# Kernel tuning notes

Hardware: AMD Instinct MI355X
Metric: run time of the kernel (lower is better)

Reference implementation:

```python
import jax, jax.numpy as jnp
import numpy as np

B, F, U, A, H = 8192, 1024, 256, 16, 8  # batch, in_features, units_layer, num_actions, hidden(=8)


def _coagent_layer(x, W0, b0, W1, b1, W2, b2):
    # x: [B, f_in]; stacked weights for U independent tiny MLPs (grouped GEMMs)
    h = jax.nn.relu(jnp.einsum('bf,uhf->buh', x, W0) + b0)   # [B, U, H]
    h = jax.nn.relu(jnp.einsum('buh,ugh->bug', h, W1) + b1)  # [B, U, H]
    q = jnp.einsum('bug,uag->bua', h, W2) + b2               # [B, U, A]
    # greedy action per coagent (epsilon-greedy with greedy=True / epsilon=0)
    return jnp.argmax(q, axis=-1).astype(jnp.float32)        # [B, U]


def setup_inputs() -> dict:
    key = jax.random.key(0)
    ks = jax.random.split(key, 19)
    n = lambda k, shape, fan: (jax.random.normal(k, shape, dtype=jnp.float32)
                               / jnp.sqrt(jnp.float32(fan)))
    return {
        'state': jax.random.normal(ks[0], (B, F), dtype=jnp.float32),
        # coagent layer 0: in_features -> 8 -> 8 -> A, stacked over U units
        'W0_0': n(ks[1], (U, H, F), F), 'b0_0': jnp.zeros((U, H), jnp.float32),
        'W1_0': n(ks[2], (U, H, H), H), 'b1_0': jnp.zeros((U, H), jnp.float32),
        'W2_0': n(ks[3], (U, A, H), H), 'b2_0': jnp.zeros((U, A), jnp.float32),
        # coagent layer 1: units_layer -> 8 -> 8 -> A, stacked over U units
        'W0_1': n(ks[4], (U, H, U), U), 'b0_1': jnp.zeros((U, H), jnp.float32),
        'W1_1': n(ks[5], (U, H, H), H), 'b1_1': jnp.zeros((U, H), jnp.float32),
        'W2_1': n(ks[6], (U, A, H), H), 'b2_1': jnp.zeros((U, A), jnp.float32),
        # Policy head: units_layer -> 8 -> 8 -> 1
        'PW0': n(ks[7], (H, U), U), 'Pb0': jnp.zeros((H,), jnp.float32),
        'PW1': n(ks[8], (H, H), H), 'Pb1': jnp.zeros((H,), jnp.float32),
        'PW2': n(ks[9], (1, H), H), 'Pb2': jnp.zeros((1,), jnp.float32),
    }


def reference(state, W0_0, b0_0, W1_0, b1_0, W2_0, b2_0,
              W0_1, b0_1, W1_1, b1_1, W2_1, b2_1,
              PW0, Pb0, PW1, Pb1, PW2, Pb2):
    a0 = _coagent_layer(state, W0_0, b0_0, W1_0, b1_0, W2_0, b2_0)  # [B, U]
    a1 = _coagent_layer(a0, W0_1, b0_1, W1_1, b1_1, W2_1, b2_1)     # [B, U]
    h = jax.nn.relu(a1 @ PW0.T + Pb0)
    h = jax.nn.relu(h @ PW1.T + Pb1)
    return h @ PW2.T + Pb2  # [B, 1]
```

## Files before the change

### kernel.cpp

```cpp
#include <hip/hip_runtime.h>
#include <cstring>
#include <cstdint>

#define B_TOTAL 8192
#define F_IN    1024
#define U_UNITS 256
#define NACT    16
#define HID     8

typedef float    f32x4  __attribute__((ext_vector_type(4)));
typedef _Float16 half8  __attribute__((ext_vector_type(8)));
typedef _Float16 half4  __attribute__((ext_vector_type(4)));


__global__ __launch_bounds__(256)
void pack3_kernel(const float* __restrict__ s0, _Float16* __restrict__ d0h, _Float16* __restrict__ d0l,
                  const float* __restrict__ s1, _Float16* __restrict__ d1h, _Float16* __restrict__ d1l,
                  const float* __restrict__ s2, _Float16* __restrict__ d2h, _Float16* __restrict__ d2l)
{
    constexpr int NB0 = (B_TOTAL / 16) * (F_IN / 128);
    constexpr int NB1 = (U_UNITS * HID / 16) * (F_IN / 128);
    __shared__ float ls[16 * 132];
    int b = blockIdx.x;
    const float* src; _Float16 *dh, *dl; int K, lg;
    if (b < NB0)            { src = s0; dh = d0h; dl = d0l; K = F_IN;    lg = 3; }
    else if (b < NB0 + NB1) { b -= NB0; src = s1; dh = d1h; dl = d1l; K = F_IN; lg = 3; }
    else                    { b -= NB0 + NB1; src = s2; dh = d2h; dl = d2l; K = U_UNITS; lg = 1; }

    const int tid = threadIdx.x;
    const int mt  = b >> lg;
    const int kb  = b & ((1 << lg) - 1);
    const int r0  = mt * 16;

#pragma unroll
    for (int i = 0; i < 2; ++i) {
        const int e = tid + (i << 8);
        const int row = e >> 5;
        const int c4  = e & 31;
        f32x4 v = *reinterpret_cast<const f32x4*>(
            &src[(size_t)(r0 + row) * K + (kb << 7) + (c4 << 2)]);
        *reinterpret_cast<f32x4*>(&ls[row * 132 + (c4 << 2)]) = v;
    }
    __syncthreads();

    const int k8 = tid >> 4, r = tid & 15;
    float x[8];
#pragma unroll
    for (int j = 0; j < 8; ++j) x[j] = ls[r * 132 + (k8 << 3) + j];
    half8 h, l;
#pragma unroll
    for (int j = 0; j < 8; ++j) {
        h[j] = (_Float16)x[j];
        l[j] = (_Float16)((x[j] - (float)h[j]) * 2048.0f);
    }
    const size_t off = (((size_t)mt * (K >> 5)) + (kb << 2) + (k8 >> 2)) * 512
                     + (size_t)(((k8 & 3) << 4) + r) * 8;
    *reinterpret_cast<half8*>(&dh[off]) = h;
    *reinterpret_cast<half8*>(&dl[off]) = l;
}

constexpr int BM = 128, BN = 128;

template<int K_TOTAL, bool A_SPLIT, bool OUT_TF32>
__global__ __launch_bounds__(256, 2)
void coagent_mfma(const _Float16* __restrict__ Ahg, const _Float16* __restrict__ Alg,
                  const _Float16* __restrict__ Bhg, const _Float16* __restrict__ Blg,
                  const float* __restrict__ b0, const float* __restrict__ W1,
                  const float* __restrict__ b1, const float* __restrict__ W2,
                  const float* __restrict__ b2, void* __restrict__ outp)
{
    struct EpiBufs { float Hs[BM][65]; _Float16 ab[BM * 8]; };
    __shared__ EpiBufs sm;

    constexpr int NTK = K_TOTAL >> 5;
    constexpr size_t TS = (size_t)NTK * 512;

    const int tid  = threadIdx.x;
    const int wave = tid >> 6;
    const int lane = tid & 63;
    const int quad = lane >> 4;
    const int l15  = lane & 15;
    const int wm   = (wave >> 1) * 64;
    const int m0   = blockIdx.y * BM;
    const int n0   = blockIdx.x * BN;

    const int at = (wave >> 1) * 4;
    const int bt = (wave & 1) * 4;

    const _Float16* Ah0 = Ahg + ((size_t)((m0 >> 4) + at)) * TS + lane * 8;
    const _Float16* Al0 = A_SPLIT ? (Alg + ((size_t)((m0 >> 4) + at)) * TS + lane * 8) : nullptr;
    const _Float16* Bh0 = Bhg + ((size_t)((n0 >> 4) + bt)) * TS + lane * 8;
    const _Float16* Bl0 = Blg + ((size_t)((n0 >> 4) + bt)) * TS + lane * 8;

    f32x4 acc1[4][4];
    f32x4 acc2[4][4];
#pragma unroll
    for (int i = 0; i < 4; ++i)
#pragma unroll
        for (int j = 0; j < 4; ++j) { acc1[i][j] = {0.f,0.f,0.f,0.f}; acc2[i][j] = {0.f,0.f,0.f,0.f}; }

    for (int kt = 0; kt < NTK; ++kt) {
        const size_t ko = (size_t)kt * 512;
        half8 af[4], bf[4], xa[4], xb[4];
#pragma unroll
        for (int mt = 0; mt < 4; ++mt)
            af[mt] = *reinterpret_cast<const half8*>(Ah0 + mt * TS + ko);
#pragma unroll
        for (int nt = 0; nt < 4; ++nt)
            bf[nt] = *reinterpret_cast<const half8*>(Bh0 + nt * TS + ko);
        if (A_SPLIT) {
#pragma unroll
            for (int mt = 0; mt < 4; ++mt)
                xa[mt] = *reinterpret_cast<const half8*>(Al0 + mt * TS + ko);
        }
#pragma unroll
        for (int nt = 0; nt < 4; ++nt)
            xb[nt] = *reinterpret_cast<const half8*>(Bl0 + nt * TS + ko);

#pragma unroll
        for (int mt = 0; mt < 4; ++mt)
#pragma unroll
            for (int nt = 0; nt < 4; ++nt)
                acc1[mt][nt] = __builtin_amdgcn_mfma_f32_16x16x32_f16(af[mt], bf[nt], acc1[mt][nt], 0, 0, 0);
        if (A_SPLIT) {
#pragma unroll
            for (int mt = 0; mt < 4; ++mt)
#pragma unroll
                for (int nt = 0; nt < 4; ++nt)
                    acc2[mt][nt] = __builtin_amdgcn_mfma_f32_16x16x32_f16(xa[mt], bf[nt], acc2[mt][nt], 0, 0, 0);
        }
#pragma unroll
        for (int mt = 0; mt < 4; ++mt)
#pragma unroll
            for (int nt = 0; nt < 4; ++nt)
                acc2[mt][nt] = __builtin_amdgcn_mfma_f32_16x16x32_f16(af[mt], xb[nt], acc2[mt][nt], 0, 0, 0);
    }

    const int ubase = n0 >> 3;
    for (int half = 0; half < 2; ++half) {
        __syncthreads();
        if ((wave & 1) == half) {
#pragma unroll
            for (int mt = 0; mt < 4; ++mt)
#pragma unroll
                for (int nt = 0; nt < 4; ++nt)
#pragma unroll
                    for (int r = 0; r < 4; ++r)
                        sm.Hs[wm + mt * 16 + quad * 4 + r][nt * 16 + l15] =
                            acc1[mt][nt][r] + acc2[mt][nt][r] * (1.0f / 2048.0f);
        }
        __syncthreads();
#pragma unroll
        for (int p = 0; p < 4; ++p) {
            const int pair = (p << 8) + tid;
            const int ul = pair >> 7;
            const int bl = pair & 127;
            const int u  = __builtin_amdgcn_readfirstlane(ubase + half * 8 + ul);
            const float* __restrict__ b0u = b0 + u * 8;
            const float* __restrict__ W1u = W1 + u * 64;
            const float* __restrict__ b1u = b1 + u * 8;
            const float* __restrict__ W2u = W2 + u * 128;
            const float* __restrict__ b2u = b2 + u * 16;

            float h[HID];
#pragma unroll
            for (int j = 0; j < HID; ++j)
                h[j] = fmaxf(sm.Hs[bl][ul * 8 + j] + b0u[j], 0.f);

            float h2[HID];
#pragma unroll
            for (int g = 0; g < HID; ++g) {
                float s = b1u[g];
#pragma unroll
                for (int j = 0; j < HID; ++j)
                    s += h[j] * W1u[g * 8 + j];
                h2[g] = fmaxf(s, 0.f);
            }

            float best = b2u[0];
#pragma unroll
            for (int j = 0; j < HID; ++j) best += h2[j] * W2u[j];
            int bi = 0;
#pragma unroll
            for (int a = 1; a < NACT; ++a) {
                float s = b2u[a];
#pragma unroll
                for (int j = 0; j < HID; ++j)
                    s += h2[j] * W2u[a * 8 + j];
                if (s > best) { best = s; bi = a; }
            }

            if (OUT_TF32) {
                ((float*)outp)[(size_t)u * B_TOTAL + m0 + bl] = (float)bi;
            } else {
                sm.ab[bl * 8 + ul] = (_Float16)bi;
            }
        }
        if (!OUT_TF32) {
            __syncthreads();
            if (tid < 128) {
                float4 v = *reinterpret_cast<float4*>(&sm.ab[tid * 8]);
                const int u = ubase + half * 8;
                const int b = m0 + tid;
                const size_t off = ((size_t)(b >> 4) * 8 + (u >> 5)) * 512
                                 + (size_t)((((u >> 3) & 3) << 4) + (b & 15)) * 8;
                *reinterpret_cast<float4*>(&((_Float16*)outp)[off]) = v;
            }
        }
    }
}


constexpr int FBM = 128, FBN = 128, FBK = 16;

template<int K_TOTAL, bool X_TRANSPOSED>
__global__ __launch_bounds__(256, 2)
void coagent_kernel(const float* __restrict__ X, const float* __restrict__ W0,
                    const float* __restrict__ b0, const float* __restrict__ W1,
                    const float* __restrict__ b1, const float* __restrict__ W2,
                    const float* __restrict__ b2, float* __restrict__ outT)
{
    struct SMemGemm { float As[FBK][FBM + 4]; float Bs[FBK][FBN + 4]; };
    union SMem { SMemGemm g; float Hs[FBM][65]; };
    __shared__ SMem sm;

    const int tid = threadIdx.x;
    const int tx = tid & 15, ty = tid >> 4;
    const int m0 = blockIdx.y * FBM, n0 = blockIdx.x * FBN;

    float acc[8][8];
#pragma unroll
    for (int i = 0; i < 8; ++i)
#pragma unroll
        for (int j = 0; j < 8; ++j) acc[i][j] = 0.f;

    for (int k0 = 0; k0 < K_TOTAL; k0 += FBK) {
        __syncthreads();
        if (X_TRANSPOSED) {
#pragma unroll
            for (int l = tid; l < (FBM * FBK) / 4; l += 256) {
                const int k = l >> 5, q = l & 31;
                const float4 v = *reinterpret_cast<const float4*>(
                    &X[(size_t)(k0 + k) * B_TOTAL + m0 + 4 * q]);
                *reinterpret_cast<float4*>(&sm.g.As[k][4 * q]) = v;
            }
        } else {
#pragma unroll
            for (int l = tid; l < (FBM * FBK) / 4; l += 256) {
                const int row = l >> 2, c = l & 3;
                const float4 v = *reinterpret_cast<const float4*>(
                    &X[(size_t)(m0 + row) * K_TOTAL + k0 + 4 * c]);
                sm.g.As[4 * c + 0][row] = v.x; sm.g.As[4 * c + 1][row] = v.y;
                sm.g.As[4 * c + 2][row] = v.z; sm.g.As[4 * c + 3][row] = v.w;
            }
        }
#pragma unroll
        for (int l = tid; l < (FBN * FBK) / 4; l += 256) {
            const int row = l >> 2, c = l & 3;
            const float4 v = *reinterpret_cast<const float4*>(
                &W0[(size_t)(n0 + row) * K_TOTAL + k0 + 4 * c]);
            sm.g.Bs[4 * c + 0][row] = v.x; sm.g.Bs[4 * c + 1][row] = v.y;
            sm.g.Bs[4 * c + 2][row] = v.z; sm.g.Bs[4 * c + 3][row] = v.w;
        }
        __syncthreads();
#pragma unroll
        for (int k = 0; k < FBK; ++k) {
            float a[8], bb[8];
            *reinterpret_cast<float4*>(&a[0])  = *reinterpret_cast<float4*>(&sm.g.As[k][4 * ty]);
            *reinterpret_cast<float4*>(&a[4])  = *reinterpret_cast<float4*>(&sm.g.As[k][64 + 4 * ty]);
            *reinterpret_cast<float4*>(&bb[0]) = *reinterpret_cast<float4*>(&sm.g.Bs[k][4 * tx]);
            *reinterpret_cast<float4*>(&bb[4]) = *reinterpret_cast<float4*>(&sm.g.Bs[k][64 + 4 * tx]);
#pragma unroll
            for (int i = 0; i < 8; ++i)
#pragma unroll
                for (int j = 0; j < 8; ++j) acc[i][j] += a[i] * bb[j];
        }
    }

    const int ub_base = n0 >> 3;
    for (int half = 0; half < 2; ++half) {
        __syncthreads();
#pragma unroll
        for (int i = 0; i < 8; ++i) {
            const int row = (i < 4) ? (4 * ty + i) : (64 + 4 * ty + (i - 4));
#pragma unroll
            for (int j = 0; j < 4; ++j)
                sm.Hs[row][4 * tx + j] = acc[i][4 * half + j];
        }
        __syncthreads();
#pragma unroll
        for (int p = 0; p < 4; ++p) {
            const int pair = (p << 8) + tid;
            const int ul = pair >> 7, bl = pair & 127;
            const int u = ub_base + half * 8 + ul;
            float h[HID];
#pragma unroll
            for (int j = 0; j < HID; ++j)
                h[j] = fmaxf(sm.Hs[bl][ul * 8 + j] + b0[u * 8 + j], 0.f);
            float h2[HID];
#pragma unroll
            for (int g = 0; g < HID; ++g) {
                float s = b1[u * 8 + g];
#pragma unroll
                for (int j = 0; j < HID; ++j) s += h[j] * W1[u * 64 + g * 8 + j];
                h2[g] = fmaxf(s, 0.f);
            }
            float best = b2[u * 16];
#pragma unroll
            for (int j = 0; j < HID; ++j) best += h2[j] * W2[u * 128 + j];
            int bi = 0;
#pragma unroll
            for (int a = 1; a < NACT; ++a) {
                float s = b2[u * 16 + a];
#pragma unroll
                for (int j = 0; j < HID; ++j) s += h2[j] * W2[u * 128 + a * 8 + j];
                if (s > best) { best = s; bi = a; }
            }
            outT[(size_t)u * B_TOTAL + m0 + bl] = (float)bi;
        }
    }
}

__global__ __launch_bounds__(256)
void policy_kernel(const float* __restrict__ A1T,
                   const float* __restrict__ PW0, const float* __restrict__ Pb0,
                   const float* __restrict__ PW1, const float* __restrict__ Pb1,
                   const float* __restrict__ PW2, const float* __restrict__ Pb2,
                   float* __restrict__ out)
{
    __shared__ float part[8][32][HID + 1];
    const int tid = threadIdx.x;
    const int b32 = tid & 31;
    const int sl  = tid >> 5;
    const int b   = blockIdx.x * 32 + b32;

    float hp[HID];
#pragma unroll
    for (int j = 0; j < HID; ++j) hp[j] = 0.f;

#pragma unroll 1
    for (int q0 = 0; q0 < 32; q0 += 8) {
        float v[8];
#pragma unroll
        for (int t = 0; t < 8; ++t)
            v[t] = A1T[(size_t)(sl * 32 + q0 + t) * B_TOTAL + b];
#pragma unroll
        for (int t = 0; t < 8; ++t)
#pragma unroll
            for (int j = 0; j < HID; ++j)
                hp[j] += v[t] * PW0[j * U_UNITS + sl * 32 + q0 + t];
    }
#pragma unroll
    for (int j = 0; j < HID; ++j) part[sl][b32][j] = hp[j];
    __syncthreads();

    if (sl == 0) {
        float h[HID];
#pragma unroll
        for (int j = 0; j < HID; ++j) {
            float s = Pb0[j];
#pragma unroll
            for (int s8 = 0; s8 < 8; ++s8) s += part[s8][b32][j];
            h[j] = fmaxf(s, 0.f);
        }
        float h2[HID];
#pragma unroll
        for (int g = 0; g < HID; ++g) {
            float s = Pb1[g];
#pragma unroll
            for (int j = 0; j < HID; ++j) s += h[j] * PW1[g * 8 + j];
            h2[g] = fmaxf(s, 0.f);
        }
        float o = Pb2[0];
#pragma unroll
        for (int j = 0; j < HID; ++j) o += h2[j] * PW2[j];
        out[b] = o;
    }
}


extern "C" void kernel_launch(void* const* d_in, const int* in_sizes, int n_in,
                              void* d_out, int out_size, void* d_ws, size_t ws_size,
                              hipStream_t stream)
{
    const float* state = (const float*)d_in[0];
    const float* W0_0  = (const float*)d_in[1];
    const float* b0_0  = (const float*)d_in[2];
    const float* W1_0  = (const float*)d_in[3];
    const float* b1_0  = (const float*)d_in[4];
    const float* W2_0  = (const float*)d_in[5];
    const float* b2_0  = (const float*)d_in[6];
    const float* W0_1  = (const float*)d_in[7];
    const float* b0_1  = (const float*)d_in[8];
    const float* W1_1  = (const float*)d_in[9];
    const float* b1_1  = (const float*)d_in[10];
    const float* W2_1  = (const float*)d_in[11];
    const float* b2_1  = (const float*)d_in[12];
    const float* PW0   = (const float*)d_in[13];
    const float* Pb0   = (const float*)d_in[14];
    const float* PW1   = (const float*)d_in[15];
    const float* Pb1   = (const float*)d_in[16];
    const float* PW2   = (const float*)d_in[17];
    const float* Pb2   = (const float*)d_in[18];

    const size_t SZ_STATE = (size_t)B_TOTAL * F_IN;
    const size_t SZ_W00   = (size_t)U_UNITS * HID * F_IN;
    const size_t SZ_W01   = (size_t)U_UNITS * HID * U_UNITS;
    const size_t NEED = (2 * SZ_STATE + 2 * SZ_W00 + 2 * SZ_W01
                         + (size_t)B_TOTAL * U_UNITS) * 2
                        + (size_t)U_UNITS * B_TOTAL * 4;

    if (ws_size >= NEED) {
        char* p = (char*)d_ws;
        _Float16* state_h = (_Float16*)p;                p += SZ_STATE * 2;
        _Float16* state_l = (_Float16*)p;                p += SZ_STATE * 2;
        _Float16* w00_h   = (_Float16*)p;                p += SZ_W00 * 2;
        _Float16* w00_l   = (_Float16*)p;                p += SZ_W00 * 2;
        _Float16* w01_h   = (_Float16*)p;                p += SZ_W01 * 2;
        _Float16* w01_l   = (_Float16*)p;                p += SZ_W01 * 2;
        _Float16* a0      = (_Float16*)p;                p += (size_t)B_TOTAL * U_UNITS * 2;
        float*    a1T     = (float*)p;

        constexpr int NB0 = (B_TOTAL / 16) * (F_IN / 128);
        constexpr int NB1 = (U_UNITS * HID / 16) * (F_IN / 128);
        constexpr int NB2 = (U_UNITS * HID / 16) * (U_UNITS / 128);
        pack3_kernel<<<NB0 + NB1 + NB2, 256, 0, stream>>>(
            state, state_h, state_l, W0_0, w00_h, w00_l, W0_1, w01_h, w01_l);

        dim3 grid((U_UNITS * HID) / BN, B_TOTAL / BM);

        coagent_mfma<F_IN, true, false><<<grid, 256, 0, stream>>>(
            state_h, state_l, w00_h, w00_l, b0_0, W1_0, b1_0, W2_0, b2_0, (void*)a0);

        coagent_mfma<U_UNITS, false, true><<<grid, 256, 0, stream>>>(
            a0, nullptr, w01_h, w01_l, b0_1, W1_1, b1_1, W2_1, b2_1, (void*)a1T);

        policy_kernel<<<B_TOTAL / 32, 256, 0, stream>>>(
            a1T, PW0, Pb0, PW1, Pb1, PW2, Pb2, (float*)d_out);
    } else {
        float* a0T = (float*)d_ws;
        float* a1T = a0T + (size_t)U_UNITS * B_TOTAL;
        dim3 grid((U_UNITS * HID) / FBN, B_TOTAL / FBM);
        coagent_kernel<F_IN, false><<<grid, 256, 0, stream>>>(
            state, W0_0, b0_0, W1_0, b1_0, W2_0, b2_0, a0T);
        coagent_kernel<U_UNITS, true><<<grid, 256, 0, stream>>>(
            a0T, W0_1, b0_1, W1_1, b1_1, W2_1, b2_1, a1T);
        policy_kernel<<<B_TOTAL / 32, 256, 0, stream>>>(
            a1T, PW0, Pb0, PW1, Pb1, PW2, Pb2, (float*)d_out);
    }
}
```

Baseline: 325.4 us.

## Double-buffer MFMA operand loads with register prefetch of the next K tile

The K loop of the grouped coagent GEMM is restructured into a two-stage register pipeline. High-half operands for tile k+1 are loaded into alternate register sets while the MFMAs for tile k run, and low-half operands are reloaded right after their last use. The loop is manually unrolled by two with `#pragma unroll 1`. The aim is to hide global-load latency behind MFMA work, at the cost of more live VGPRs. The final iteration also prefetches one tile past the end of K, which may read past the end of the buffer.

```diff
diff --git a/kernel.cpp b/kernel.cpp
--- a/kernel.cpp
+++ b/kernel.cpp
@@ -61,6 +61,46 @@
 
 constexpr int BM = 128, BN = 128;
 
+#define KSTEP(HA_C, HB_C, HA_N, HB_N, KN)                                      \
+    {                                                                          \
+        const size_t kn_ = (size_t)(KN) * 512;                                 \
+        _Pragma("unroll")                                                      \
+        for (int mt = 0; mt < 4; ++mt)                                         \
+            HA_N[mt] = *reinterpret_cast<const half8*>(Ah0 + mt * TS + kn_);   \
+        _Pragma("unroll")                                                      \
+        for (int nt = 0; nt < 4; ++nt)                                         \
+            HB_N[nt] = *reinterpret_cast<const half8*>(Bh0 + nt * TS + kn_);   \
+                                                    \
+        _Pragma("unroll")                                                      \
+        for (int mt = 0; mt < 4; ++mt)                                         \
+            _Pragma("unroll")                                                  \
+            for (int nt = 0; nt < 4; ++nt)                                     \
+                acc1[mt][nt] = __builtin_amdgcn_mfma_f32_16x16x32_f16(         \
+                    HA_C[mt], HB_C[nt], acc1[mt][nt], 0, 0, 0);                \
+                           \
+        if constexpr (A_SPLIT) {                                               \
+            _Pragma("unroll")                                                  \
+            for (int mt = 0; mt < 4; ++mt)                                     \
+                _Pragma("unroll")                                              \
+                for (int nt = 0; nt < 4; ++nt)                                 \
+                    acc2[mt][nt] = __builtin_amdgcn_mfma_f32_16x16x32_f16(     \
+                        lA[mt], HB_C[nt], acc2[mt][nt], 0, 0, 0);              \
+            _Pragma("unroll")                                                  \
+            for (int mt = 0; mt < 4; ++mt)                                     \
+                lA[mt] = *reinterpret_cast<const half8*>(Al0 + mt * TS + kn_); \
+        }                                                                      \
+                           \
+        _Pragma("unroll")                                                      \
+        for (int mt = 0; mt < 4; ++mt)                                         \
+            _Pragma("unroll")                                                  \
+            for (int nt = 0; nt < 4; ++nt)                                     \
+                acc2[mt][nt] = __builtin_amdgcn_mfma_f32_16x16x32_f16(         \
+                    HA_C[mt], lB[nt], acc2[mt][nt], 0, 0, 0);                  \
+        _Pragma("unroll")                                                      \
+        for (int nt = 0; nt < 4; ++nt)                                         \
+            lB[nt] = *reinterpret_cast<const half8*>(Bl0 + nt * TS + kn_);     \
+    }
+
 template<int K_TOTAL, bool A_SPLIT, bool OUT_TF32>
 __global__ __launch_bounds__(256, 2)
 void coagent_mfma(const _Float16* __restrict__ Ahg, const _Float16* __restrict__ Alg,
@@ -99,41 +139,27 @@
 #pragma unroll
         for (int j = 0; j < 4; ++j) { acc1[i][j] = {0.f,0.f,0.f,0.f}; acc2[i][j] = {0.f,0.f,0.f,0.f}; }
 
-    for (int kt = 0; kt < NTK; ++kt) {
-        const size_t ko = (size_t)kt * 512;
-        half8 af[4], bf[4], xa[4], xb[4];
+    half8 hA0[4], hB0[4], hA1[4], hB1[4], lA[4], lB[4];
+
+#pragma unroll
+    for (int mt = 0; mt < 4; ++mt)
+        hA0[mt] = *reinterpret_cast<const half8*>(Ah0 + mt * TS);
+#pragma unroll
+    for (int nt = 0; nt < 4; ++nt)
+        hB0[nt] = *reinterpret_cast<const half8*>(Bh0 + nt * TS);
+    if constexpr (A_SPLIT) {
 #pragma unroll
         for (int mt = 0; mt < 4; ++mt)
-            af[mt] = *reinterpret_cast<const half8*>(Ah0 + mt * TS + ko);
-#pragma unroll
-        for (int nt = 0; nt < 4; ++nt)
-            bf[nt] = *reinterpret_cast<const half8*>(Bh0 + nt * TS + ko);
-        if (A_SPLIT) {
-#pragma unroll
-            for (int mt = 0; mt < 4; ++mt)
-                xa[mt] = *reinterpret_cast<const half8*>(Al0 + mt * TS + ko);
-        }
-#pragma unroll
-        for (int nt = 0; nt < 4; ++nt)
-            xb[nt] = *reinterpret_cast<const half8*>(Bl0 + nt * TS + ko);
-
-#pragma unroll
-        for (int mt = 0; mt < 4; ++mt)
-#pragma unroll
-            for (int nt = 0; nt < 4; ++nt)
-                acc1[mt][nt] = __builtin_amdgcn_mfma_f32_16x16x32_f16(af[mt], bf[nt], acc1[mt][nt], 0, 0, 0);
-        if (A_SPLIT) {
-#pragma unroll
-            for (int mt = 0; mt < 4; ++mt)
-#pragma unroll
-                for (int nt = 0; nt < 4; ++nt)
-                    acc2[mt][nt] = __builtin_amdgcn_mfma_f32_16x16x32_f16(xa[mt], bf[nt], acc2[mt][nt], 0, 0, 0);
-        }
-#pragma unroll
-        for (int mt = 0; mt < 4; ++mt)
-#pragma unroll
-            for (int nt = 0; nt < 4; ++nt)
-                acc2[mt][nt] = __builtin_amdgcn_mfma_f32_16x16x32_f16(af[mt], xb[nt], acc2[mt][nt], 0, 0, 0);
+            lA[mt] = *reinterpret_cast<const half8*>(Al0 + mt * TS);
+    }
+#pragma unroll
+    for (int nt = 0; nt < 4; ++nt)
+        lB[nt] = *reinterpret_cast<const half8*>(Bl0 + nt * TS);
+
+#pragma unroll 1
+    for (int kt = 0; kt < NTK; kt += 2) {
+        KSTEP(hA0, hB0, hA1, hB1, kt + 1)
+        KSTEP(hA1, hB1, hA0, hB0, kt + 2)
     }
 
     const int ubase = n0 >> 3;
```

Measured after the change: 307.5 us. -5.5%, faster.

## Stage MFMA operand tiles through double-buffered LDS with direct global-to-LDS loads

Applied to the files above, without the earlier changes.

Each of the four waves now issues global_load_lds copies for one operand slab (A hi, A lo, B hi, B lo) into a double-buffered shared-memory stage. All waves then read their MFMA fragments from LDS instead of each wave reloading shared A/B tiles from global memory. The next K-tile is prefetched while the current one is computed, and a barrier now ends every iteration. Block indices are also remapped with a swizzle to improve L2 locality. In exchange the kernel uses 64 KB of LDS per block, which may limit occupancy, and the swizzle hardcodes a 16x64 grid.

```diff
diff --git a/kernel.cpp b/kernel.cpp
--- a/kernel.cpp
+++ b/kernel.cpp
@@ -12,6 +12,14 @@
 typedef _Float16 half8  __attribute__((ext_vector_type(8)));
 typedef _Float16 half4  __attribute__((ext_vector_type(4)));
 
+
+__device__ __forceinline__ void gload_lds16(const _Float16* g, _Float16* l)
+{
+    __builtin_amdgcn_global_load_lds(
+        (const __attribute__((address_space(1))) void*)g,
+        (__attribute__((address_space(3))) void*)l,
+        16, 0, 0);
+}
 
 __global__ __launch_bounds__(256)
 void pack3_kernel(const float* __restrict__ s0, _Float16* __restrict__ d0h, _Float16* __restrict__ d0l,
@@ -70,7 +78,8 @@
                   const float* __restrict__ b2, void* __restrict__ outp)
 {
     struct EpiBufs { float Hs[BM][65]; _Float16 ab[BM * 8]; };
-    __shared__ EpiBufs sm;
+    union SMemU { _Float16 stage[2][16384]; EpiBufs epi; };
+    __shared__ SMemU sm;
 
     constexpr int NTK = K_TOTAL >> 5;
     constexpr size_t TS = (size_t)NTK * 512;
@@ -81,16 +90,20 @@
     const int quad = lane >> 4;
     const int l15  = lane & 15;
     const int wm   = (wave >> 1) * 64;
-    const int m0   = blockIdx.y * BM;
-    const int n0   = blockIdx.x * BN;
+
+    const int flat = blockIdx.y * 16 + blockIdx.x;
+    const int vid  = (flat & 7) * 128 + (flat >> 3);
+    const int m0   = (vid & 63) * BM;
+    const int n0   = (vid >> 6) * BN;
 
     const int at = (wave >> 1) * 4;
     const int bt = (wave & 1) * 4;
 
-    const _Float16* Ah0 = Ahg + ((size_t)((m0 >> 4) + at)) * TS + lane * 8;
-    const _Float16* Al0 = A_SPLIT ? (Alg + ((size_t)((m0 >> 4) + at)) * TS + lane * 8) : nullptr;
-    const _Float16* Bh0 = Bhg + ((size_t)((n0 >> 4) + bt)) * TS + lane * 8;
-    const _Float16* Bl0 = Blg + ((size_t)((n0 >> 4) + bt)) * TS + lane * 8;
+    const _Float16* greg = Ahg; int tb = m0 >> 4;
+    if (wave == 1)      { greg = A_SPLIT ? Alg : Ahg; }
+    else if (wave == 2) { greg = Bhg; tb = n0 >> 4; }
+    else if (wave == 3) { greg = Blg; tb = n0 >> 4; }
+    const _Float16* gbase = greg + (size_t)tb * TS + lane * 8;
 
     f32x4 acc1[4][4];
     f32x4 acc2[4][4];
@@ -99,41 +112,60 @@
 #pragma unroll
         for (int j = 0; j < 4; ++j) { acc1[i][j] = {0.f,0.f,0.f,0.f}; acc2[i][j] = {0.f,0.f,0.f,0.f}; }
 
+    if (A_SPLIT || wave != 1) {
+#pragma unroll
+        for (int i = 0; i < 8; ++i)
+            gload_lds16(gbase + (size_t)i * TS, &sm.stage[0][(wave * 8 + i) * 512]);
+    }
+    __syncthreads();
+
+    int cur = 0;
+#pragma unroll 1
     for (int kt = 0; kt < NTK; ++kt) {
-        const size_t ko = (size_t)kt * 512;
-        half8 af[4], bf[4], xa[4], xb[4];
+        if (kt + 1 < NTK && (A_SPLIT || wave != 1)) {
+            const _Float16* g = gbase + (size_t)(kt + 1) * 512;
+#pragma unroll
+            for (int i = 0; i < 8; ++i)
+                gload_lds16(g + (size_t)i * TS, &sm.stage[cur ^ 1][(wave * 8 + i) * 512]);
+        }
+
+        const _Float16* SB = sm.stage[cur];
+        half8 af[4], bf[4], la[4], lb[4];
 #pragma unroll
         for (int mt = 0; mt < 4; ++mt)
-            af[mt] = *reinterpret_cast<const half8*>(Ah0 + mt * TS + ko);
+            af[mt] = *reinterpret_cast<const half8*>(&SB[(at + mt) * 512 + lane * 8]);
 #pragma unroll
         for (int nt = 0; nt < 4; ++nt)
-            bf[nt] = *reinterpret_cast<const half8*>(Bh0 + nt * TS + ko);
-        if (A_SPLIT) {
+            bf[nt] = *reinterpret_cast<const half8*>(&SB[8192 + (bt + nt) * 512 + lane * 8]);
+        if constexpr (A_SPLIT) {
 #pragma unroll
             for (int mt = 0; mt < 4; ++mt)
-                xa[mt] = *reinterpret_cast<const half8*>(Al0 + mt * TS + ko);
+                la[mt] = *reinterpret_cast<const half8*>(&SB[4096 + (at + mt) * 512 + lane * 8]);
         }
 #pragma unroll
         for (int nt = 0; nt < 4; ++nt)
-            xb[nt] = *reinterpret_cast<const half8*>(Bl0 + nt * TS + ko);
+            lb[nt] = *reinterpret_cast<const half8*>(&SB[12288 + (bt + nt) * 512 + lane * 8]);
 
 #pragma unroll
         for (int mt = 0; mt < 4; ++mt)
 #pragma unroll
             for (int nt = 0; nt < 4; ++nt)
                 acc1[mt][nt] = __builtin_amdgcn_mfma_f32_16x16x32_f16(af[mt], bf[nt], acc1[mt][nt], 0, 0, 0);
-        if (A_SPLIT) {
+        if constexpr (A_SPLIT) {
 #pragma unroll
             for (int mt = 0; mt < 4; ++mt)
 #pragma unroll
                 for (int nt = 0; nt < 4; ++nt)
-                    acc2[mt][nt] = __builtin_amdgcn_mfma_f32_16x16x32_f16(xa[mt], bf[nt], acc2[mt][nt], 0, 0, 0);
+                    acc2[mt][nt] = __builtin_amdgcn_mfma_f32_16x16x32_f16(la[mt], bf[nt], acc2[mt][nt], 0, 0, 0);
         }
 #pragma unroll
         for (int mt = 0; mt < 4; ++mt)
 #pragma unroll
             for (int nt = 0; nt < 4; ++nt)
-                acc2[mt][nt] = __builtin_amdgcn_mfma_f32_16x16x32_f16(af[mt], xb[nt], acc2[mt][nt], 0, 0, 0);
+                acc2[mt][nt] = __builtin_amdgcn_mfma_f32_16x16x32_f16(af[mt], lb[nt], acc2[mt][nt], 0, 0, 0);
+
+        __syncthreads();
+        cur ^= 1;
     }
 
     const int ubase = n0 >> 3;
@@ -146,7 +178,7 @@
                 for (int nt = 0; nt < 4; ++nt)
 #pragma unroll
                     for (int r = 0; r < 4; ++r)
-                        sm.Hs[wm + mt * 16 + quad * 4 + r][nt * 16 + l15] =
+                        sm.epi.Hs[wm + mt * 16 + quad * 4 + r][nt * 16 + l15] =
                             acc1[mt][nt][r] + acc2[mt][nt][r] * (1.0f / 2048.0f);
         }
         __syncthreads();
@@ -165,7 +197,7 @@
             float h[HID];
 #pragma unroll
             for (int j = 0; j < HID; ++j)
-                h[j] = fmaxf(sm.Hs[bl][ul * 8 + j] + b0u[j], 0.f);
+                h[j] = fmaxf(sm.epi.Hs[bl][ul * 8 + j] + b0u[j], 0.f);
 
             float h2[HID];
 #pragma unroll
@@ -193,13 +225,13 @@
             if (OUT_TF32) {
                 ((float*)outp)[(size_t)u * B_TOTAL + m0 + bl] = (float)bi;
             } else {
-                sm.ab[bl * 8 + ul] = (_Float16)bi;
+                sm.epi.ab[bl * 8 + ul] = (_Float16)bi;
             }
         }
         if (!OUT_TF32) {
             __syncthreads();
             if (tid < 128) {
-                float4 v = *reinterpret_cast<float4*>(&sm.ab[tid * 8]);
+                float4 v = *reinterpret_cast<float4*>(&sm.epi.ab[tid * 8]);
                 const int u = ubase + half * 8;
                 const int b = m0 + tid;
                 const size_t off = ((size_t)(b >> 4) * 8 + (u >> 5)) * 512
```

After: 319.5 us. About the same (-1.8%).
